# Optimization experiments

Hardware: AMD Instinct MI355X
Metric: run time of the kernel (lower is better)

## Reference

```python
import jax, jax.numpy as jnp
import numpy as np

N = 50000        # nodes
E = 800000       # edges (avg degree 16)
IN_DIM = 256
H = 8            # heads
D = 32           # out_dim per head
T = 4            # edge_type_num
F = 16           # edge_feature_dim
NEG_SLOPE = 0.2


def setup_inputs() -> dict:
    key = jax.random.key(0)
    ks = jax.random.split(key, 9)
    feat = jax.random.normal(ks[0], (N, IN_DIM), dtype=jnp.float32)
    e_pro = jax.random.normal(ks[1], (E, F), dtype=jnp.float32)
    mask = jax.random.uniform(ks[2], (E, T), dtype=jnp.float32)
    W_n = jax.random.normal(ks[3], (IN_DIM, H * D), dtype=jnp.float32) * (1.0 / np.sqrt(IN_DIM))
    attn_l = jax.random.normal(ks[4], (H, D, T), dtype=jnp.float32) * 0.1
    attn_r = jax.random.normal(ks[5], (H, D, T), dtype=jnp.float32) * 0.1
    attn_m = jax.random.normal(ks[6], (H, F, T), dtype=jnp.float32) * 0.1
    src = jax.random.randint(ks[7], (E,), 0, N, dtype=jnp.int32)
    dst = jax.random.randint(ks[8], (E,), 0, N, dtype=jnp.int32)
    return {"feat": feat, "e_pro": e_pro, "mask": mask, "W_n": W_n,
            "attn_l": attn_l, "attn_r": attn_r, "attn_m": attn_m,
            "src": src, "dst": dst}


def reference(feat, e_pro, mask, W_n, attn_l, attn_r, attn_m, src, dst):
    # node projection: [N, H, D]
    feat_src = (feat @ W_n).reshape(N, H, D)

    # per-node attention logits per edge type: [N, H, T]
    el = jnp.einsum("nhd,hdt->nht", feat_src, attn_l)
    er = jnp.einsum("nhd,hdt->nht", feat_src, attn_r)
    # per-edge logits per edge type: [E, H, T]
    em = jnp.einsum("ef,hft->eht", e_pro, attn_m)

    # bmm with edge-type mask [E, T] -> scalar per head: [E, H]
    left = jnp.einsum("eht,et->eh", el[src], mask)
    right = jnp.einsum("eht,et->eh", er[dst], mask)
    em_e = jnp.einsum("eht,et->eh", em, mask)

    e = (left + right + em_e) / 3.0
    e = jnp.where(e > 0, e, NEG_SLOPE * e)  # leaky_relu

    # edge softmax over incoming edges of each dst node (stable)
    e_max = jax.ops.segment_max(e, dst, num_segments=N)          # [N, H]
    e_exp = jnp.exp(e - e_max[dst])                               # [E, H]
    e_sum = jax.ops.segment_sum(e_exp, dst, num_segments=N)      # [N, H]
    a = e_exp / e_sum[dst]                                       # [E, H]

    # u_mul_e + sum aggregation: [E, H, D] -> [N, H, D]
    msg = feat_src[src] * a[:, :, None]
    rst = jax.ops.segment_sum(msg, dst, num_segments=N)

    # cat=True: concat heads
    return rst.reshape(N, H * D)
```

## Files before the change

kernel.cpp:

```cpp
#include <hip/hip_runtime.h>
#include <hip/hip_bf16.h>
#include <hip/hip_fp16.h>

#define NN 50000
#define NEDGE 800000
#define INDIM 256
#define NH 8
#define ND 32
#define HD 256
#define NT 4
#define NF 16

typedef __attribute__((ext_vector_type(8))) short s16x8;
typedef __attribute__((ext_vector_type(4))) float f32x4;
typedef unsigned short u16;

__device__ __forceinline__ float bf2f(u16 u) {
    return __uint_as_float(((unsigned int)u) << 16);
}
__device__ __forceinline__ u16 f2bf(float f) {
    __hip_bfloat16 h = __float2bfloat16(f);
    return *reinterpret_cast<u16*>(&h);
}
__device__ __forceinline__ u16 f2h(float f) {
    __half h = __float2half(f);
    return *reinterpret_cast<u16*>(&h);
}
__device__ __forceinline__ float h2f(u16 u) {
    __half h = *reinterpret_cast<__half*>(&u);
    return __half2float(h);
}

__global__ __launch_bounds__(256) void prep_kernel(const float* __restrict__ W,
                                                   u16* __restrict__ Wt,
                                                   int* __restrict__ cnt,
                                                   int* __restrict__ cursor)
{
    int idx = blockIdx.x * 256 + threadIdx.x;
    int k = idx >> 8, c = idx & 255;
    Wt[(size_t)c * 256 + k] = f2bf(W[idx]);
    if (idx < NN) { cnt[idx] = 0; cursor[idx] = 0; }
}

__global__ __launch_bounds__(256) void gemm_mfma(
    const float* __restrict__ feat, const u16* __restrict__ Wt,
    const int* __restrict__ dst, int* __restrict__ cnt,
    u16* __restrict__ fs, int nrows)
{
    const int tid = threadIdx.x;
    {
        int e0 = (blockIdx.x * 256 + tid) * 2;
        if (e0 < NEDGE)     atomicAdd(&cnt[dst[e0]], 1);
        if (e0 + 1 < NEDGE) atomicAdd(&cnt[dst[e0 + 1]], 1);
    }

    __shared__ u16 At[32 * 256];
    const int brow = blockIdx.x * 32;

    #pragma unroll
    for (int it = 0; it < 4; ++it) {
        int fo = it * 2048 + tid * 8;
        int row = fo >> 8, col = fo & 255;
        int grow = brow + row;
        if (grow >= nrows) grow = nrows - 1;
        const float* gp = feat + (size_t)grow * 256 + col;
        float4 x = *reinterpret_cast<const float4*>(gp);
        float4 y = *reinterpret_cast<const float4*>(gp + 4);
        s16x8 v;
        v[0] = (short)f2bf(x.x); v[1] = (short)f2bf(x.y);
        v[2] = (short)f2bf(x.z); v[3] = (short)f2bf(x.w);
        v[4] = (short)f2bf(y.x); v[5] = (short)f2bf(y.y);
        v[6] = (short)f2bf(y.z); v[7] = (short)f2bf(y.w);
        int byte = (col * 2) ^ ((row & 7) << 4);
        *reinterpret_cast<s16x8*>((char*)At + row * 512 + byte) = v;
    }
    __syncthreads();

    const int wave = tid >> 6, lane = tid & 63;
    const int c0 = wave * 64;
    const int rA = lane & 15;
    const int kg = lane >> 4;

    f32x4 acc[2][4] = {};

    for (int k0 = 0; k0 < 256; k0 += 32) {
        const int kk = k0 + kg * 8;
        const int byte = (kk * 2) ^ ((rA & 7) << 4);
        s16x8 a0 = *reinterpret_cast<const s16x8*>((char*)At + rA * 512 + byte);
        s16x8 a1 = *reinterpret_cast<const s16x8*>((char*)At + (16 + rA) * 512 + byte);
        #pragma unroll
        for (int ct = 0; ct < 4; ++ct) {
            s16x8 b = *reinterpret_cast<const s16x8*>(Wt + (size_t)(c0 + ct * 16 + rA) * 256 + kk);
            acc[0][ct] = __builtin_amdgcn_mfma_f32_16x16x32_bf16(a0, b, acc[0][ct], 0, 0, 0);
            acc[1][ct] = __builtin_amdgcn_mfma_f32_16x16x32_bf16(a1, b, acc[1][ct], 0, 0, 0);
        }
    }

    #pragma unroll
    for (int rt = 0; rt < 2; ++rt) {
        #pragma unroll
        for (int r = 0; r < 4; ++r) {
            int row = brow + rt * 16 + kg * 4 + r;
            if (row < nrows) {
                #pragma unroll
                for (int ct = 0; ct < 4; ++ct) {
                    fs[(size_t)row * 256 + c0 + ct * 16 + rA] = f2bf(acc[rt][ct][r]);
                }
            }
        }
    }
}

__global__ void scan1_kernel(const int* __restrict__ cnt, int* __restrict__ off,
                             int* __restrict__ blksum, int n) {
    __shared__ int sm[256];
    int i = blockIdx.x * 256 + threadIdx.x;
    int v = (i < n) ? cnt[i] : 0;
    sm[threadIdx.x] = v;
    __syncthreads();
    for (int d = 1; d < 256; d <<= 1) {
        int t = (threadIdx.x >= d) ? sm[threadIdx.x - d] : 0;
        __syncthreads();
        sm[threadIdx.x] += t;
        __syncthreads();
    }
    if (i < n) off[i] = sm[threadIdx.x] - v;
    if (threadIdx.x == 255) blksum[blockIdx.x] = sm[255];
}

__global__ void scan2_kernel(int* blksum, int nb) {
    __shared__ int sm[256];
    int v = (threadIdx.x < nb) ? blksum[threadIdx.x] : 0;
    sm[threadIdx.x] = v;
    __syncthreads();
    for (int d = 1; d < 256; d <<= 1) {
        int t = (threadIdx.x >= d) ? sm[threadIdx.x - d] : 0;
        __syncthreads();
        sm[threadIdx.x] += t;
        __syncthreads();
    }
    blksum[threadIdx.x] = sm[threadIdx.x] - v;
}

__global__ void scan3_kernel(int* __restrict__ off, const int* __restrict__ blksum,
                             int n, int ne) {
    int i = blockIdx.x * 256 + threadIdx.x;
    if (i < n) off[i] += blksum[blockIdx.x];
    if (i == 0) off[n] = ne;
}

__global__ __launch_bounds__(256) void elr_kernel(
    const u16* __restrict__ fs,
    const float* __restrict__ attn_l, const float* __restrict__ attn_r,
    u16* __restrict__ el, u16* __restrict__ er,
    const int* __restrict__ dst, const int* __restrict__ off,
    int* __restrict__ cursor, int* __restrict__ eIdx,
    int n, int ne)
{
    __shared__ float s_al[NH * ND * NT];
    __shared__ float s_ar[NH * ND * NT];

    int gid = blockIdx.x * 256 + threadIdx.x;
    bool doFill = gid < ne;
    int fd = 0;
    if (doFill) fd = dst[gid];

    for (int i = threadIdx.x; i < NH * ND * NT; i += 256) {
        s_al[i] = attn_l[i];
        s_ar[i] = attn_r[i];
    }
    __syncthreads();
    int wv = threadIdx.x >> 6, lane = threadIdx.x & 63;
    int node = blockIdx.x * 4 + wv;
    if (node < n) {
        int h = lane >> 3, j0 = (lane & 7) * 4;
        ushort4 u = *reinterpret_cast<const ushort4*>(fs + (size_t)node * HD + lane * 4);
        float f0 = bf2f(u.x), f1 = bf2f(u.y), f2 = bf2f(u.z), f3 = bf2f(u.w);
        const float* al = s_al + h * (ND * NT) + j0 * NT;
        const float* ar = s_ar + h * (ND * NT) + j0 * NT;
        float pl[NT], pr[NT];
        #pragma unroll
        for (int t = 0; t < NT; ++t) {
            pl[t] = f0*al[t] + f1*al[NT + t] + f2*al[2*NT + t] + f3*al[3*NT + t];
            pr[t] = f0*ar[t] + f1*ar[NT + t] + f2*ar[2*NT + t] + f3*ar[3*NT + t];
        }
        #pragma unroll
        for (int d = 1; d < 8; d <<= 1) {
            #pragma unroll
            for (int t = 0; t < NT; ++t) {
                pl[t] += __shfl_xor(pl[t], d);
                pr[t] += __shfl_xor(pr[t], d);
            }
        }
        if ((lane & 7) == 0) {
            ushort4 ol, orr;
            ol.x = f2h(pl[0]); ol.y = f2h(pl[1]); ol.z = f2h(pl[2]); ol.w = f2h(pl[3]);
            orr.x = f2h(pr[0]); orr.y = f2h(pr[1]); orr.z = f2h(pr[2]); orr.w = f2h(pr[3]);
            *reinterpret_cast<ushort4*>(el + (size_t)node * (NH*NT) + h * NT) = ol;
            *reinterpret_cast<ushort4*>(er + (size_t)node * (NH*NT) + h * NT) = orr;
        }
    }

    if (doFill) {
        int p = atomicAdd(&cursor[fd], 1);
        eIdx[off[fd] + p] = gid;
    }
}

__global__ __launch_bounds__(256) void edge_kernel(
    const float* __restrict__ e_pro, const float* __restrict__ mask,
    const float* __restrict__ attn_m,
    const int* __restrict__ src, const int* __restrict__ dst,
    const u16* __restrict__ el, const u16* __restrict__ er,
    u16* __restrict__ ev, int ne)
{
    __shared__ float4 s_am4[NF][NH];
    __shared__ float s_ep[32][17];
    __shared__ float s_mk[32][5];
    const int tid = threadIdx.x;
    const int eb = blockIdx.x * 32;

    for (int i = tid; i < NH * NF; i += 256) {
        int h = i >> 4, f = i & 15;
        const float* p = attn_m + (size_t)h * (NF * NT) + f * NT;
        s_am4[f][h] = make_float4(p[0], p[1], p[2], p[3]);
    }
    {
        int f2i = tid * 2;
        float2 v = *reinterpret_cast<const float2*>(e_pro + (size_t)eb * NF + f2i);
        int e_l = f2i >> 4, f = f2i & 15;
        s_ep[e_l][f] = v.x; s_ep[e_l][f + 1] = v.y;
    }
    if (tid < 128) {
        s_mk[tid >> 2][tid & 3] = mask[(size_t)eb * NT + tid];
    }
    __syncthreads();

    int e = eb + (tid >> 3);
    const int el_ = tid >> 3 & 31;
    const int j = tid & 7;

    int s = src[e], d = dst[e];
    float4 mk = make_float4(s_mk[el_][0], s_mk[el_][1], s_mk[el_][2], s_mk[el_][3]);

    union { uint2 v; u16 u[4]; } lv, rv;
    lv.v = *reinterpret_cast<const uint2*>(el + (size_t)s * (NH*NT) + j * NT);
    rv.v = *reinterpret_cast<const uint2*>(er + (size_t)d * (NH*NT) + j * NT);

    float em = 0.f;
    #pragma unroll
    for (int f = 0; f < NF; ++f) {
        float4 am = s_am4[f][j];
        float amm = mk.x*am.x + mk.y*am.y + mk.z*am.z + mk.w*am.w;
        em = fmaf(s_ep[el_][f], amm, em);
    }
    float left  = mk.x*h2f(lv.u[0]) + mk.y*h2f(lv.u[1]) + mk.z*h2f(lv.u[2]) + mk.w*h2f(lv.u[3]);
    float right = mk.x*h2f(rv.u[0]) + mk.y*h2f(rv.u[1]) + mk.z*h2f(rv.u[2]) + mk.w*h2f(rv.u[3]);

    float v = (left + right + em) * (1.0f / 3.0f);
    v = v > 0.f ? v : 0.2f * v;
    ev[(size_t)e * NH + j] = f2h(__expf(v));
}

__global__ __launch_bounds__(256) void agg_kernel(
    const int* __restrict__ off, const int* __restrict__ eIdx,
    const int* __restrict__ src, const u16* __restrict__ ev,
    const u16* __restrict__ fs, float* __restrict__ out, int n)
{
    int wv = threadIdx.x >> 6, lane = threadIdx.x & 63;
    int node = blockIdx.x * 4 + wv;
    if (node >= n) return;
    int beg = off[node], end = off[node + 1];
    int deg = end - beg;

    int h = lane & 7, sub = lane >> 3;
    float vc[8];
    int sc[8];
    float s = 0.f;
    #pragma unroll
    for (int slot = 0; slot < 8; ++slot) {
        int i = beg + slot * 8 + sub;
        float v = 0.f; int sn = 0;
        if (i < end) {
            int e = eIdx[i];
            v = h2f(ev[(size_t)e * NH + h]);
            sn = src[e];
        }
        vc[slot] = v; sc[slot] = sn; s += v;
    }
    for (int i = beg + 64 + sub; i < end; i += 8) {
        int e = eIdx[i];
        s += h2f(ev[(size_t)e * NH + h]);
    }
    s += __shfl_xor(s, 8);
    s += __shfl_xor(s, 16);
    s += __shfl_xor(s, 32);

    int h2 = lane >> 3;
    float S = __shfl(s, h2);
    float invS = S > 0.f ? 1.f / S : 0.f;
    const int col = lane * 4;
    float a0 = 0.f, a1 = 0.f, a2 = 0.f, a3 = 0.f;
    int deg_ = deg < 64 ? deg : 64;
    int nchunk = (deg_ + 7) >> 3;
    #pragma unroll
    for (int c = 0; c < 8; ++c) {
        if (c >= nchunk) break;
        float w8 = vc[c];
        int s8 = sc[c];
        #pragma unroll
        for (int q = 0; q < 8; ++q) {
            float w = __shfl(w8, q * 8 + h2);
            int sn  = __shfl(s8, q * 8 + h2);
            ushort4 u = *reinterpret_cast<const ushort4*>(fs + (size_t)sn * HD + col);
            a0 = fmaf(w, bf2f(u.x), a0); a1 = fmaf(w, bf2f(u.y), a1);
            a2 = fmaf(w, bf2f(u.z), a2); a3 = fmaf(w, bf2f(u.w), a3);
        }
    }
    for (int i = beg + 64; i < end; ++i) {
        int e = eIdx[i];
        float w = h2f(ev[(size_t)e * NH + h2]);
        int sn = src[e];
        ushort4 u = *reinterpret_cast<const ushort4*>(fs + (size_t)sn * HD + col);
        a0 = fmaf(w, bf2f(u.x), a0); a1 = fmaf(w, bf2f(u.y), a1);
        a2 = fmaf(w, bf2f(u.z), a2); a3 = fmaf(w, bf2f(u.w), a3);
    }
    a0 *= invS; a1 *= invS; a2 *= invS; a3 *= invS;
    *reinterpret_cast<float4*>(&out[(size_t)node * HD + col]) = make_float4(a0, a1, a2, a3);
}

extern "C" void kernel_launch(void* const* d_in, const int* in_sizes, int n_in,
                              void* d_out, int out_size, void* d_ws, size_t ws_size,
                              hipStream_t stream)
{
    const float* feat   = (const float*)d_in[0];
    const float* e_pro  = (const float*)d_in[1];
    const float* mask   = (const float*)d_in[2];
    const float* W_n    = (const float*)d_in[3];
    const float* attn_l = (const float*)d_in[4];
    const float* attn_r = (const float*)d_in[5];
    const float* attn_m = (const float*)d_in[6];
    const int* src      = (const int*)d_in[7];
    const int* dst      = (const int*)d_in[8];
    float* out = (float*)d_out;

    char* ws = (char*)d_ws;
    size_t o = 0;
    auto alloc = [&](size_t bytes) -> void* {
        void* p = (void*)(ws + o);
        o += (bytes + 255) & ~(size_t)255;
        return p;
    };
    u16* fs     = (u16*)alloc((size_t)NN * HD * 2);
    u16* Wt     = (u16*)alloc((size_t)INDIM * HD * 2);
    u16* el     = (u16*)alloc((size_t)NN * NH * NT * 2);
    u16* er     = (u16*)alloc((size_t)NN * NH * NT * 2);
    u16* ev     = (u16*)alloc((size_t)NEDGE * NH * 2);
    int* eIdx   = (int*)alloc((size_t)NEDGE * 4);
    int* cnt    = (int*)alloc((size_t)NN * 4);
    int* cursor = (int*)alloc((size_t)NN * 4);
    int* offs   = (int*)alloc((size_t)(NN + 1) * 4);
    int* blksum = (int*)alloc(256 * 4);
    (void)ws_size; (void)in_sizes; (void)n_in; (void)out_size;

    dim3 b256(256);
    hipLaunchKernelGGL(prep_kernel, dim3(256), b256, 0, stream, W_n, Wt, cnt, cursor);
    hipLaunchKernelGGL(gemm_mfma, dim3((NN + 31) / 32), b256, 0, stream, feat, Wt, dst, cnt, fs, NN);
    hipLaunchKernelGGL(scan1_kernel, dim3((NN + 255) / 256), b256, 0, stream, cnt, offs, blksum, NN);
    hipLaunchKernelGGL(scan2_kernel, dim3(1), b256, 0, stream, blksum, (NN + 255) / 256);
    hipLaunchKernelGGL(scan3_kernel, dim3((NN + 255) / 256), b256, 0, stream, offs, blksum, NN, NEDGE);
    hipLaunchKernelGGL(elr_kernel, dim3((NN + 3) / 4), b256, 0, stream,
                       fs, attn_l, attn_r, el, er, dst, offs, cursor, eIdx, NN, NEDGE);
    hipLaunchKernelGGL(edge_kernel, dim3(NEDGE / 32), b256, 0, stream,
                       e_pro, mask, attn_m, src, dst, el, er, ev, NEDGE);
    hipLaunchKernelGGL(agg_kernel, dim3((NN + 3) / 4), b256, 0, stream,
                       offs, eIdx, src, ev, fs, out, NN);
}
```

Baseline: 253.5 us.

## Move edge counting before GEMM and fuse CSR fill into GEMM kernel

Degree counting moves into the prep kernel, with memsets zeroing the counters, and the scan now runs before the GEMM. The GEMM kernel then does the CSR edge-index fill (cursor atomics and eIdx scatter) alongside its tile loads, and elr_kernel only computes attention logits. The aim is to hide the scattered atomic and store latency behind GEMM memory traffic and to slim elr_kernel. It costs two memset launches and a larger prep grid, and the atomics may slow the GEMM's load phase.

New measurement: 263.5 us. 1.04x slower.

```diff
diff --git a/kernel.cpp b/kernel.cpp
--- a/kernel.cpp
+++ b/kernel.cpp
@@ -33,26 +33,67 @@
 
 __global__ __launch_bounds__(256) void prep_kernel(const float* __restrict__ W,
                                                    u16* __restrict__ Wt,
-                                                   int* __restrict__ cnt,
-                                                   int* __restrict__ cursor)
+                                                   const int* __restrict__ dst,
+                                                   int* __restrict__ cnt)
 {
     int idx = blockIdx.x * 256 + threadIdx.x;
-    int k = idx >> 8, c = idx & 255;
-    Wt[(size_t)c * 256 + k] = f2bf(W[idx]);
-    if (idx < NN) { cnt[idx] = 0; cursor[idx] = 0; }
+    if (idx < 65536) {
+        int k = idx >> 8, c = idx & 255;
+        Wt[(size_t)c * 256 + k] = f2bf(W[idx]);
+    }
+    if (idx < NEDGE) atomicAdd(&cnt[dst[idx]], 1);
+}
+
+__global__ void scan1_kernel(const int* __restrict__ cnt, int* __restrict__ off,
+                             int* __restrict__ blksum, int n) {
+    __shared__ int sm[256];
+    int i = blockIdx.x * 256 + threadIdx.x;
+    int v = (i < n) ? cnt[i] : 0;
+    sm[threadIdx.x] = v;
+    __syncthreads();
+    for (int d = 1; d < 256; d <<= 1) {
+        int t = (threadIdx.x >= d) ? sm[threadIdx.x - d] : 0;
+        __syncthreads();
+        sm[threadIdx.x] += t;
+        __syncthreads();
+    }
+    if (i < n) off[i] = sm[threadIdx.x] - v;
+    if (threadIdx.x == 255) blksum[blockIdx.x] = sm[255];
+}
+
+__global__ void scan2_kernel(int* blksum, int nb) {
+    __shared__ int sm[256];
+    int v = (threadIdx.x < nb) ? blksum[threadIdx.x] : 0;
+    sm[threadIdx.x] = v;
+    __syncthreads();
+    for (int d = 1; d < 256; d <<= 1) {
+        int t = (threadIdx.x >= d) ? sm[threadIdx.x - d] : 0;
+        __syncthreads();
+        sm[threadIdx.x] += t;
+        __syncthreads();
+    }
+    blksum[threadIdx.x] = sm[threadIdx.x] - v;
+}
+
+__global__ void scan3_kernel(int* __restrict__ off, const int* __restrict__ blksum,
+                             int n, int ne) {
+    int i = blockIdx.x * 256 + threadIdx.x;
+    if (i < n) off[i] += blksum[blockIdx.x];
+    if (i == 0) off[n] = ne;
 }
 
 __global__ __launch_bounds__(256) void gemm_mfma(
     const float* __restrict__ feat, const u16* __restrict__ Wt,
-    const int* __restrict__ dst, int* __restrict__ cnt,
+    const int* __restrict__ dst, const int* __restrict__ off,
+    int* __restrict__ cursor, int* __restrict__ eIdx,
     u16* __restrict__ fs, int nrows)
 {
     const int tid = threadIdx.x;
-    {
-        int e0 = (blockIdx.x * 256 + tid) * 2;
-        if (e0 < NEDGE)     atomicAdd(&cnt[dst[e0]], 1);
-        if (e0 + 1 < NEDGE) atomicAdd(&cnt[dst[e0 + 1]], 1);
-    }
+
+    int e0 = (blockIdx.x * 256 + tid) * 2;
+    int d0 = -1, d1 = -1;
+    if (e0 < NEDGE)     d0 = dst[e0];
+    if (e0 + 1 < NEDGE) d1 = dst[e0 + 1];
 
     __shared__ u16 At[32 * 256];
     const int brow = blockIdx.x * 32;
@@ -74,6 +115,14 @@
         int byte = (col * 2) ^ ((row & 7) << 4);
         *reinterpret_cast<s16x8*>((char*)At + row * 512 + byte) = v;
     }
+
+    {
+        int o0 = 0, o1 = 0;
+        if (d0 >= 0) o0 = off[d0];
+        if (d1 >= 0) o1 = off[d1];
+        if (d0 >= 0) { int p = atomicAdd(&cursor[d0], 1); eIdx[o0 + p] = e0; }
+        if (d1 >= 0) { int p = atomicAdd(&cursor[d1], 1); eIdx[o1 + p] = e0 + 1; }
+    }
     __syncthreads();
 
     const int wave = tid >> 6, lane = tid & 63;
@@ -111,60 +160,13 @@
     }
 }
 
-__global__ void scan1_kernel(const int* __restrict__ cnt, int* __restrict__ off,
-                             int* __restrict__ blksum, int n) {
-    __shared__ int sm[256];
-    int i = blockIdx.x * 256 + threadIdx.x;
-    int v = (i < n) ? cnt[i] : 0;
-    sm[threadIdx.x] = v;
-    __syncthreads();
-    for (int d = 1; d < 256; d <<= 1) {
-        int t = (threadIdx.x >= d) ? sm[threadIdx.x - d] : 0;
-        __syncthreads();
-        sm[threadIdx.x] += t;
-        __syncthreads();
-    }
-    if (i < n) off[i] = sm[threadIdx.x] - v;
-    if (threadIdx.x == 255) blksum[blockIdx.x] = sm[255];
-}
-
-__global__ void scan2_kernel(int* blksum, int nb) {
-    __shared__ int sm[256];
-    int v = (threadIdx.x < nb) ? blksum[threadIdx.x] : 0;
-    sm[threadIdx.x] = v;
-    __syncthreads();
-    for (int d = 1; d < 256; d <<= 1) {
-        int t = (threadIdx.x >= d) ? sm[threadIdx.x - d] : 0;
-        __syncthreads();
-        sm[threadIdx.x] += t;
-        __syncthreads();
-    }
-    blksum[threadIdx.x] = sm[threadIdx.x] - v;
-}
-
-__global__ void scan3_kernel(int* __restrict__ off, const int* __restrict__ blksum,
-                             int n, int ne) {
-    int i = blockIdx.x * 256 + threadIdx.x;
-    if (i < n) off[i] += blksum[blockIdx.x];
-    if (i == 0) off[n] = ne;
-}
-
 __global__ __launch_bounds__(256) void elr_kernel(
     const u16* __restrict__ fs,
     const float* __restrict__ attn_l, const float* __restrict__ attn_r,
-    u16* __restrict__ el, u16* __restrict__ er,
-    const int* __restrict__ dst, const int* __restrict__ off,
-    int* __restrict__ cursor, int* __restrict__ eIdx,
-    int n, int ne)
+    u16* __restrict__ el, u16* __restrict__ er, int n)
 {
     __shared__ float s_al[NH * ND * NT];
     __shared__ float s_ar[NH * ND * NT];
-
-    int gid = blockIdx.x * 256 + threadIdx.x;
-    bool doFill = gid < ne;
-    int fd = 0;
-    if (doFill) fd = dst[gid];
-
     for (int i = threadIdx.x; i < NH * ND * NT; i += 256) {
         s_al[i] = attn_l[i];
         s_ar[i] = attn_r[i];
@@ -172,38 +174,32 @@
     __syncthreads();
     int wv = threadIdx.x >> 6, lane = threadIdx.x & 63;
     int node = blockIdx.x * 4 + wv;
-    if (node < n) {
-        int h = lane >> 3, j0 = (lane & 7) * 4;
-        ushort4 u = *reinterpret_cast<const ushort4*>(fs + (size_t)node * HD + lane * 4);
-        float f0 = bf2f(u.x), f1 = bf2f(u.y), f2 = bf2f(u.z), f3 = bf2f(u.w);
-        const float* al = s_al + h * (ND * NT) + j0 * NT;
-        const float* ar = s_ar + h * (ND * NT) + j0 * NT;
-        float pl[NT], pr[NT];
+    if (node >= n) return;
+    int h = lane >> 3, j0 = (lane & 7) * 4;
+    ushort4 u = *reinterpret_cast<const ushort4*>(fs + (size_t)node * HD + lane * 4);
+    float f0 = bf2f(u.x), f1 = bf2f(u.y), f2 = bf2f(u.z), f3 = bf2f(u.w);
+    const float* al = s_al + h * (ND * NT) + j0 * NT;
+    const float* ar = s_ar + h * (ND * NT) + j0 * NT;
+    float pl[NT], pr[NT];
+    #pragma unroll
+    for (int t = 0; t < NT; ++t) {
+        pl[t] = f0*al[t] + f1*al[NT + t] + f2*al[2*NT + t] + f3*al[3*NT + t];
+        pr[t] = f0*ar[t] + f1*ar[NT + t] + f2*ar[2*NT + t] + f3*ar[3*NT + t];
+    }
+    #pragma unroll
+    for (int d = 1; d < 8; d <<= 1) {
         #pragma unroll
         for (int t = 0; t < NT; ++t) {
-            pl[t] = f0*al[t] + f1*al[NT + t] + f2*al[2*NT + t] + f3*al[3*NT + t];
-            pr[t] = f0*ar[t] + f1*ar[NT + t] + f2*ar[2*NT + t] + f3*ar[3*NT + t];
-        }
-        #pragma unroll
-        for (int d = 1; d < 8; d <<= 1) {
-            #pragma unroll
-            for (int t = 0; t < NT; ++t) {
-                pl[t] += __shfl_xor(pl[t], d);
-                pr[t] += __shfl_xor(pr[t], d);
-            }
-        }
-        if ((lane & 7) == 0) {
-            ushort4 ol, orr;
-            ol.x = f2h(pl[0]); ol.y = f2h(pl[1]); ol.z = f2h(pl[2]); ol.w = f2h(pl[3]);
-            orr.x = f2h(pr[0]); orr.y = f2h(pr[1]); orr.z = f2h(pr[2]); orr.w = f2h(pr[3]);
-            *reinterpret_cast<ushort4*>(el + (size_t)node * (NH*NT) + h * NT) = ol;
-            *reinterpret_cast<ushort4*>(er + (size_t)node * (NH*NT) + h * NT) = orr;
-        }
-    }
-
-    if (doFill) {
-        int p = atomicAdd(&cursor[fd], 1);
-        eIdx[off[fd] + p] = gid;
+            pl[t] += __shfl_xor(pl[t], d);
+            pr[t] += __shfl_xor(pr[t], d);
+        }
+    }
+    if ((lane & 7) == 0) {
+        ushort4 ol, orr;
+        ol.x = f2h(pl[0]); ol.y = f2h(pl[1]); ol.z = f2h(pl[2]); ol.w = f2h(pl[3]);
+        orr.x = f2h(pr[0]); orr.y = f2h(pr[1]); orr.z = f2h(pr[2]); orr.w = f2h(pr[3]);
+        *reinterpret_cast<ushort4*>(el + (size_t)node * (NH*NT) + h * NT) = ol;
+        *reinterpret_cast<ushort4*>(er + (size_t)node * (NH*NT) + h * NT) = orr;
     }
 }
 
@@ -364,13 +360,16 @@
     (void)ws_size; (void)in_sizes; (void)n_in; (void)out_size;
 
     dim3 b256(256);
-    hipLaunchKernelGGL(prep_kernel, dim3(256), b256, 0, stream, W_n, Wt, cnt, cursor);
-    hipLaunchKernelGGL(gemm_mfma, dim3((NN + 31) / 32), b256, 0, stream, feat, Wt, dst, cnt, fs, NN);
+    hipMemsetAsync(cnt, 0, (size_t)NN * 4, stream);
+    hipMemsetAsync(cursor, 0, (size_t)NN * 4, stream);
+    hipLaunchKernelGGL(prep_kernel, dim3((NEDGE + 255) / 256), b256, 0, stream, W_n, Wt, dst, cnt);
     hipLaunchKernelGGL(scan1_kernel, dim3((NN + 255) / 256), b256, 0, stream, cnt, offs, blksum, NN);
     hipLaunchKernelGGL(scan2_kernel, dim3(1), b256, 0, stream, blksum, (NN + 255) / 256);
     hipLaunchKernelGGL(scan3_kernel, dim3((NN + 255) / 256), b256, 0, stream, offs, blksum, NN, NEDGE);
+    hipLaunchKernelGGL(gemm_mfma, dim3((NN + 31) / 32), b256, 0, stream,
+                       feat, Wt, dst, offs, cursor, eIdx, fs, NN);
     hipLaunchKernelGGL(elr_kernel, dim3((NN + 3) / 4), b256, 0, stream,
-                       fs, attn_l, attn_r, el, er, dst, offs, cursor, eIdx, NN, NEDGE);
+                       fs, attn_l, attn_r, el, er, NN);
     hipLaunchKernelGGL(edge_kernel, dim3(NEDGE / 32), b256, 0, stream,
                        e_pro, mask, attn_m, src, dst, el, er, ev, NEDGE);
     hipLaunchKernelGGL(agg_kernel, dim3((NN + 3) / 4), b256, 0, stream,
```
